# Kernel optimization log

Hardware: AMD Instinct MI355X
Metric: run time of the kernel (lower is better)

## Reference

```python
import jax, jax.numpy as jnp
import numpy as np

B, T, C, H = 2, 2048, 2048, 16
HD = C // H  # head dim = 128
ROPE_BASE = 10000.0


def apply_rope(x):
    # x: [B, T, H, HD]; interleaved-pair rotation as in torchtune RoPE
    t = x.shape[1]
    half = x.shape[-1] // 2
    theta = 1.0 / (ROPE_BASE ** (jnp.arange(0, HD, 2, dtype=jnp.float32) / HD))  # [HD/2]
    ang = jnp.arange(t, dtype=jnp.float32)[:, None] * theta[None, :]  # [T, HD/2]
    cos = jnp.cos(ang)[None, :, None, :]  # [1, T, 1, HD/2]
    sin = jnp.sin(ang)[None, :, None, :]
    xs = x.reshape(*x.shape[:-1], half, 2)  # [B,T,H,HD/2,2]
    x0, x1 = xs[..., 0], xs[..., 1]
    out = jnp.stack([x0 * cos - x1 * sin, x1 * cos + x0 * sin], axis=-1)
    return out.reshape(x.shape)


def setup_inputs() -> dict:
    key = jax.random.key(0)
    k1, k2, k3 = jax.random.split(key, 3)
    x = jax.random.normal(k1, (B, T, C), dtype=jnp.float32)
    attn_mask = jnp.tril(jnp.ones((T, T), dtype=bool))[None, None]  # causal [1,1,T,T]
    W_attn = jax.random.normal(k2, (3 * C, C), dtype=jnp.float32) * (C ** -0.5)
    W_proj = jax.random.normal(k3, (C, C), dtype=jnp.float32) * (C ** -0.5)
    return {"x": x, "attn_mask": attn_mask, "W_attn": W_attn, "W_proj": W_proj}


def reference(x, attn_mask, W_attn, W_proj):
    b, t, c = x.shape
    qkv = x @ W_attn.T  # [B,T,3C]
    q, k, v = jnp.split(qkv, 3, axis=-1)
    q = apply_rope(q.reshape(b, t, H, HD)).transpose(0, 2, 1, 3)  # [B,H,T,HD]
    k = apply_rope(k.reshape(b, t, H, HD)).transpose(0, 2, 1, 3)
    v = v.reshape(b, t, H, HD).transpose(0, 2, 1, 3)
    scale = 1.0 / jnp.sqrt(jnp.float32(HD))
    scores = jnp.einsum("bhqd,bhkd->bhqk", q, k) * scale
    scores = jnp.where(attn_mask, scores, jnp.finfo(scores.dtype).min)
    probs = jax.nn.softmax(scores, axis=-1)
    y = jnp.einsum("bhqk,bhkd->bhqd", probs, v)  # [B,H,T,HD]
    y = y.transpose(0, 2, 1, 3).reshape(b, t, c)
    return y @ W_proj.T
```

## Files before the change

kernel.cpp:

```cpp
#include <hip/hip_runtime.h>
#include <hip/hip_bf16.h>
#include <math.h>

typedef unsigned short u16;
typedef unsigned int   u32;
typedef __attribute__((ext_vector_type(8)))  short bf16x8;
typedef __attribute__((ext_vector_type(4)))  float f32x4;
typedef __attribute__((ext_vector_type(16))) float f32x16;

#define B_  2
#define T_  2048
#define C_  2048
#define H_  16
#define HD_ 128
#define M_  4096
#define N3C 6144

__device__ __forceinline__ float bf2f_lo(u32 u) { return __uint_as_float(u << 16); }
__device__ __forceinline__ float bf2f_hi(u32 u) { return __uint_as_float(u & 0xffff0000u); }

__device__ __forceinline__ u16 f2bf(float f) {
    u32 u = __float_as_uint(f);
    return (u16)((u + 0x7fffu + ((u >> 16) & 1u)) >> 16);
}
__device__ __forceinline__ u32 pack2(float a, float b) {
    return (u32)f2bf(a) | ((u32)f2bf(b) << 16);
}
__device__ __forceinline__ void store1(float* p, float v) { *p = v; }
__device__ __forceinline__ void store1(__hip_bfloat16* p, float v) { *(u16*)p = f2bf(v); }

__device__ __forceinline__ void gload16(const void* g, void* l) {
    __builtin_amdgcn_global_load_lds((__attribute__((address_space(1))) void*)g,
                                     (__attribute__((address_space(3))) void*)l, 16, 0, 0);
}

__global__ __launch_bounds__(256) void cvt_bf16(const float* __restrict__ in,
                                                u16* __restrict__ out, int n8) {
    const int i = blockIdx.x * 256 + threadIdx.x;
    if (i < n8) {
        const float4 a = ((const float4*)in)[2 * i];
        const float4 b = ((const float4*)in)[2 * i + 1];
        ((uint4*)out)[i] = make_uint4(pack2(a.x, a.y), pack2(a.z, a.w),
                                      pack2(b.x, b.y), pack2(b.z, b.w));
    }
}

template <typename TO>
__global__ __launch_bounds__(256) void gemm_lds(const __hip_bfloat16* __restrict__ A,
                                                const __hip_bfloat16* __restrict__ W,
                                                TO* __restrict__ Cout,
                                                int N, int K, int gx) {
    __shared__ u16 As[128 * 32];
    __shared__ u16 Bs[128 * 32];
    const int nwg = gridDim.x * gridDim.y;
    const int id  = blockIdx.y * gx + blockIdx.x;
    const int swz = (id & 7) * (nwg >> 3) + (id >> 3);
    const int bm  = (swz / gx) * 128;
    const int bn  = (swz % gx) * 128;

    const int tid  = threadIdx.x;
    const int w    = tid >> 6;
    const int lane = tid & 63;
    const int g    = lane >> 4;
    const int c    = lane & 15;
    const int wr   = (w >> 1) * 64;
    const int wc   = (w & 1) * 64;

    const int srow = lane >> 2;
    const int scol = (lane & 3) * 8;
    const __hip_bfloat16* ga0 = A + (size_t)(bm + w * 32 + srow) * K + scol;
    const __hip_bfloat16* ga1 = ga0 + (size_t)16 * K;
    const __hip_bfloat16* gb0 = W + (size_t)(bn + w * 32 + srow) * K + scol;
    const __hip_bfloat16* gb1 = gb0 + (size_t)16 * K;
    u16* la0 = &As[(w * 32) * 32];
    u16* la1 = &As[(w * 32 + 16) * 32];
    u16* lb0 = &Bs[(w * 32) * 32];
    u16* lb1 = &Bs[(w * 32 + 16) * 32];

    f32x4 acc[4][4];
#pragma unroll
    for (int mi = 0; mi < 4; ++mi)
#pragma unroll
        for (int ni = 0; ni < 4; ++ni)
            acc[mi][ni] = (f32x4){0.f, 0.f, 0.f, 0.f};

    for (int k0 = 0; k0 < K; k0 += 32) {
        __syncthreads();
        gload16(ga0 + k0, la0);
        gload16(ga1 + k0, la1);
        gload16(gb0 + k0, lb0);
        gload16(gb1 + k0, lb1);
        __syncthreads();

        bf16x8 af[4], bfr[4];
#pragma unroll
        for (int mi = 0; mi < 4; ++mi)
            af[mi] = *(const bf16x8*)&As[(wr + mi * 16 + c) * 32 + g * 8];
#pragma unroll
        for (int ni = 0; ni < 4; ++ni)
            bfr[ni] = *(const bf16x8*)&Bs[(wc + ni * 16 + c) * 32 + g * 8];
#pragma unroll
        for (int mi = 0; mi < 4; ++mi)
#pragma unroll
            for (int ni = 0; ni < 4; ++ni)
                acc[mi][ni] = __builtin_amdgcn_mfma_f32_16x16x32_bf16(
                    af[mi], bfr[ni], acc[mi][ni], 0, 0, 0);
    }

#pragma unroll
    for (int mi = 0; mi < 4; ++mi)
#pragma unroll
        for (int ni = 0; ni < 4; ++ni)
#pragma unroll
            for (int i = 0; i < 4; ++i) {
                const int row = bm + wr + mi * 16 + 4 * g + i;
                const int col = bn + wc + ni * 16 + c;
                store1(Cout + (size_t)row * N + col, acc[mi][ni][i]);
            }
}

__device__ __forceinline__ void stage_tile(u16* dst, const float* src, int ldk, int tid) {
    const int r0  = tid >> 3;
    const int off = (tid & 7) * 4;
#pragma unroll
    for (int it = 0; it < 4; ++it) {
        const int row = r0 + it * 32;
        const float4 v = *(const float4*)(src + (size_t)row * ldk + off);
        *(uint2*)&dst[row * 40 + off] = make_uint2(pack2(v.x, v.y), pack2(v.z, v.w));
    }
}
__device__ __forceinline__ void stage_tile(u16* dst, const __hip_bfloat16* src, int ldk, int tid) {
    const int r0  = tid >> 2;
    const int off = (tid & 3) * 8;
#pragma unroll
    for (int it = 0; it < 2; ++it) {
        const int row = r0 + it * 64;
        *(uint4*)&dst[row * 40 + off] = *(const uint4*)(src + (size_t)row * ldk + off);
    }
}

template <typename TA, typename TW, typename TO>
__global__ __launch_bounds__(256) void gemm_mfma(const TA* __restrict__ A,
                                                 const TW* __restrict__ W,
                                                 TO* __restrict__ Cout,
                                                 int N, int K, int gx) {
    __shared__ u16 As[128 * 40];
    __shared__ u16 Bs[128 * 40];
    const int nwg = gridDim.x * gridDim.y;
    const int id  = blockIdx.y * gx + blockIdx.x;
    const int swz = (id & 7) * (nwg >> 3) + (id >> 3);
    const int bm  = (swz / gx) * 128;
    const int bn  = (swz % gx) * 128;

    const int tid  = threadIdx.x;
    const int w    = tid >> 6;
    const int lane = tid & 63;
    const int g    = lane >> 4;
    const int c    = lane & 15;
    const int wr   = (w >> 1) * 64;
    const int wc   = (w & 1) * 64;

    f32x4 acc[4][4];
#pragma unroll
    for (int mi = 0; mi < 4; ++mi)
#pragma unroll
        for (int ni = 0; ni < 4; ++ni)
            acc[mi][ni] = (f32x4){0.f, 0.f, 0.f, 0.f};

    const TA* Ab = A + (size_t)bm * K;
    const TW* Wb = W + (size_t)bn * K;

    for (int k0 = 0; k0 < K; k0 += 32) {
        __syncthreads();
        stage_tile(As, Ab + k0, K, tid);
        stage_tile(Bs, Wb + k0, K, tid);
        __syncthreads();

        bf16x8 af[4], bfr[4];
#pragma unroll
        for (int mi = 0; mi < 4; ++mi)
            af[mi] = *(const bf16x8*)&As[(wr + mi * 16 + c) * 40 + g * 8];
#pragma unroll
        for (int ni = 0; ni < 4; ++ni)
            bfr[ni] = *(const bf16x8*)&Bs[(wc + ni * 16 + c) * 40 + g * 8];
#pragma unroll
        for (int mi = 0; mi < 4; ++mi)
#pragma unroll
            for (int ni = 0; ni < 4; ++ni)
                acc[mi][ni] = __builtin_amdgcn_mfma_f32_16x16x32_bf16(
                    af[mi], bfr[ni], acc[mi][ni], 0, 0, 0);
    }

#pragma unroll
    for (int mi = 0; mi < 4; ++mi)
#pragma unroll
        for (int ni = 0; ni < 4; ++ni)
#pragma unroll
            for (int i = 0; i < 4; ++i) {
                const int row = bm + wr + mi * 16 + 4 * g + i;
                const int col = bn + wc + ni * 16 + c;
                store1(Cout + (size_t)row * N + col, acc[mi][ni][i]);
            }
}

__global__ __launch_bounds__(256) void rope_kernel(__hip_bfloat16* __restrict__ qkv) {
    const int id  = blockIdx.x * 256 + threadIdx.x;
    const int i   = id & 63;
    const int h   = (id >> 6) & (H_ - 1);
    const int qk  = (id >> 10) & 1;
    const int row = id >> 11;
    const int t   = row & (T_ - 1);
    const size_t base = (size_t)row * N3C + (size_t)qk * C_ + h * HD_ + 2 * i;
    u32* p = (u32*)((u16*)qkv + base);
    const u32 v = *p;
    const float x0 = bf2f_lo(v), x1 = bf2f_hi(v);
    const float l2th = 0.20762050593046f;
    const float theta = exp2f(-(float)i * l2th);
    const float ang = (float)t * theta;
    float s, cc;
    sincosf(ang, &s, &cc);
    *p = pack2(x0 * cc - x1 * s, x1 * cc + x0 * s);
}

__device__ __forceinline__ int PI_(int s) {
    return (s & 51) | ((s & 4) << 1) | ((s & 8) >> 1);
}

__global__ __launch_bounds__(256, 2) void attn_mfma2(const __hip_bfloat16* __restrict__ qkv,
                                                     __hip_bfloat16* __restrict__ y) {
    __shared__ u16 Ks[64 * 136];
    __shared__ u16 Vt[128 * 72];
    __shared__ float Red[128];

    const int tid  = threadIdx.x;
    const int w    = tid >> 6;
    const int lane = tid & 63;
    const int c31  = lane & 31;
    const int hi   = lane >> 5;
    const int bid  = blockIdx.x;
    const int bh   = bid & 31;
    const int qb   = 15 - (bid >> 5);
    const int b    = bh >> 4, h = bh & 15;
    const int q0   = qb * 128;

    const size_t base = (size_t)b * T_ * N3C + (size_t)h * HD_;
    const __hip_bfloat16* Qp = qkv + base;
    const __hip_bfloat16* Kp = qkv + base + C_;
    const __hip_bfloat16* Vp = qkv + base + 2 * C_;

    bf16x8 qf[8];
    {
        const size_t qoff = (size_t)(q0 + w * 32 + c31) * N3C + hi * 8;
#pragma unroll
        for (int kc = 0; kc < 8; ++kc)
            qf[kc] = *(const bf16x8*)(Qp + qoff + kc * 16);
    }

    f32x16 o[4];
#pragma unroll
    for (int db = 0; db < 4; ++db)
#pragma unroll
        for (int r = 0; r < 16; ++r) o[db][r] = 0.f;

    float m_ = -1e30f, l_ = 0.f;
    const int   myq   = q0 + w * 32 + c31;
    const float SCALE = 0.08838834764831845f;

    const int s_   = tid >> 2;
    const int dsub = tid & 3;
    const int vcol = PI_(s_) ^ (dsub << 4);

    const int nkt = 2 * qb + 2;
    for (int kt = 0; kt < nkt; ++kt) {
        const int k0 = kt * 64;
        __syncthreads();
#pragma unroll
        for (int it = 0; it < 4; ++it) {
            const int col = dsub * 32 + it * 8;
            const size_t goff = (size_t)(k0 + s_) * N3C + col;
            *(uint4*)&Ks[s_ * 136 + col] = *(const uint4*)(Kp + goff);
            const uint4 vv = *(const uint4*)(Vp + goff);
            const u32 vw[4] = {vv.x, vv.y, vv.z, vv.w};
#pragma unroll
            for (int j = 0; j < 8; ++j)
                Vt[(col + j) * 72 + vcol] = (u16)(vw[j >> 1] >> ((j & 1) * 16));
        }
        __syncthreads();

        f32x16 sA, sB;
#pragma unroll
        for (int r = 0; r < 16; ++r) { sA[r] = 0.f; sB[r] = 0.f; }
#pragma unroll
        for (int kc = 0; kc < 8; ++kc) {
            const bf16x8 ka = *(const bf16x8*)&Ks[c31 * 136 + kc * 16 + hi * 8];
            sA = __builtin_amdgcn_mfma_f32_32x32x16_bf16(ka, qf[kc], sA, 0, 0, 0);
            const bf16x8 kb_ = *(const bf16x8*)&Ks[(32 + c31) * 136 + kc * 16 + hi * 8];
            sB = __builtin_amdgcn_mfma_f32_32x32x16_bf16(kb_, qf[kc], sB, 0, 0, 0);
        }

        float pmax = -1e30f;
#pragma unroll
        for (int r = 0; r < 16; ++r) {
            const int cr = (r & 3) + 8 * (r >> 2) + 4 * hi;
            sA[r] = (k0 + cr      <= myq) ? sA[r] * SCALE : -1e30f;
            sB[r] = (k0 + 32 + cr <= myq) ? sB[r] * SCALE : -1e30f;
            pmax = fmaxf(pmax, fmaxf(sA[r], sB[r]));
        }
        pmax = fmaxf(pmax, __shfl_xor(pmax, 32));

        if (__any(pmax > m_ + 8.f)) {
            const float mn   = fmaxf(m_, pmax);
            const float corr = __expf(m_ - mn);
            Red[w * 32 + c31] = corr;
            float cf[16];
#pragma unroll
            for (int r = 0; r < 16; ++r)
                cf[r] = Red[w * 32 + ((r & 3) + 8 * (r >> 2) + 4 * hi)];
#pragma unroll
            for (int db = 0; db < 4; ++db)
#pragma unroll
                for (int r = 0; r < 16; ++r) o[db][r] *= cf[r];
            l_ *= corr;
            m_ = mn;
        }

        float psum = 0.f;
#pragma unroll
        for (int r = 0; r < 16; ++r) {
            sA[r] = __expf(sA[r] - m_); psum += sA[r];
            sB[r] = __expf(sB[r] - m_); psum += sB[r];
        }
        psum += __shfl_xor(psum, 32);
        l_ += psum;

#pragma unroll
        for (int kb2 = 0; kb2 < 2; ++kb2) {
#pragma unroll
            for (int c2 = 0; c2 < 2; ++c2) {
                union { u32 u[4]; bf16x8 v; } pk;
#pragma unroll
                for (int q2 = 0; q2 < 4; ++q2) {
                    const int r = 8 * c2 + 2 * q2;
                    const float e0 = kb2 ? sB[r]     : sA[r];
                    const float e1 = kb2 ? sB[r + 1] : sA[r + 1];
                    pk.u[q2] = pack2(e0, e1);
                }
#pragma unroll
                for (int db = 0; db < 4; ++db) {
                    const int colb = (kb2 * 32 + c2 * 16 + hi * 8) ^ (db << 4);
                    const bf16x8 vb = *(const bf16x8*)&Vt[(db * 32 + c31) * 72 + colb];
                    o[db] = __builtin_amdgcn_mfma_f32_32x32x16_bf16(pk.v, vb, o[db], 0, 0, 0);
                }
            }
        }
    }

    Red[w * 32 + c31] = l_;
    float lv[16];
#pragma unroll
    for (int r = 0; r < 16; ++r)
        lv[r] = 1.f / Red[w * 32 + ((r & 3) + 8 * (r >> 2) + 4 * hi)];
#pragma unroll
    for (int db = 0; db < 4; ++db)
#pragma unroll
        for (int r = 0; r < 16; ++r) {
            const int q = q0 + w * 32 + (r & 3) + 8 * (r >> 2) + 4 * hi;
            store1(y + (size_t)(b * T_ + q) * C_ + h * HD_ + db * 32 + c31,
                   o[db][r] * lv[r]);
        }
}

extern "C" void kernel_launch(void* const* d_in, const int* in_sizes, int n_in,
                              void* d_out, int out_size, void* d_ws, size_t ws_size,
                              hipStream_t stream) {
    const float* x  = (const float*)d_in[0];
    const float* Wa = (const float*)d_in[2];
    const float* Wp = (const float*)d_in[3];
    float* out = (float*)d_out;

    u16* ws = (u16*)d_ws;
    __hip_bfloat16* qkv = (__hip_bfloat16*)ws;
    __hip_bfloat16* y   = (__hip_bfloat16*)(ws + (size_t)M_ * N3C);

    const size_t NEED = ((size_t)M_ * N3C + (size_t)M_ * C_ +
                         (size_t)M_ * C_ +
                         (size_t)N3C * C_ + (size_t)C_ * C_) * 2;

    if (ws_size >= NEED) {
        u16* xb  = ws + (size_t)M_ * N3C + (size_t)M_ * C_;
        u16* Wab = xb + (size_t)M_ * C_;
        u16* Wpb = Wab + (size_t)N3C * C_;

        cvt_bf16<<<(M_ * C_ / 8 + 255) / 256, 256, 0, stream>>>(x, xb, M_ * C_ / 8);
        cvt_bf16<<<(N3C * C_ / 8 + 255) / 256, 256, 0, stream>>>(Wa, Wab, N3C * C_ / 8);
        cvt_bf16<<<(C_ * C_ / 8 + 255) / 256, 256, 0, stream>>>(Wp, Wpb, C_ * C_ / 8);

        gemm_lds<__hip_bfloat16>
            <<<dim3(N3C / 128, M_ / 128), 256, 0, stream>>>(
                (const __hip_bfloat16*)xb, (const __hip_bfloat16*)Wab, qkv, N3C, C_, N3C / 128);
        rope_kernel<<<(M_ * C_) / 256, 256, 0, stream>>>(qkv);
        attn_mfma2<<<512, 256, 0, stream>>>(qkv, y);
        gemm_lds<float>
            <<<dim3(C_ / 128, M_ / 128), 256, 0, stream>>>(
                y, (const __hip_bfloat16*)Wpb, out, C_, C_, C_ / 128);
    } else {
        gemm_mfma<float, float, __hip_bfloat16>
            <<<dim3(N3C / 128, M_ / 128), 256, 0, stream>>>(x, Wa, qkv, N3C, C_, N3C / 128);
        rope_kernel<<<(M_ * C_) / 256, 256, 0, stream>>>(qkv);
        attn_mfma2<<<512, 256, 0, stream>>>(qkv, y);
        gemm_mfma<__hip_bfloat16, float, float>
            <<<dim3(C_ / 128, M_ / 128), 256, 0, stream>>>(y, Wp, out, C_, C_, C_ / 128);
    }
}
```

Before: 323.0 us.

## Triple-buffer GEMM LDS loads and register-prefetch K/V tiles in attention

The GEMM becomes a three-stage LDS pipeline using async global_load_lds. Loads run two tiles ahead, synchronised by explicit vmcnt waits and a single barrier per iteration, so global latency overlaps the MFMA work. The attention kernel prefetches the next K/V tile into registers while the current tile is consumed, and raises wave priority around the MFMA blocks. The cost is more LDS (three buffers) and more registers, which may lower occupancy, and correctness now depends on the hand-placed waitcnt values matching the number of outstanding loads.

```diff
diff --git a/kernel.cpp b/kernel.cpp
--- a/kernel.cpp
+++ b/kernel.cpp
@@ -46,12 +46,12 @@
 }
 
 template <typename TO>
-__global__ __launch_bounds__(256) void gemm_lds(const __hip_bfloat16* __restrict__ A,
-                                                const __hip_bfloat16* __restrict__ W,
-                                                TO* __restrict__ Cout,
-                                                int N, int K, int gx) {
-    __shared__ u16 As[128 * 32];
-    __shared__ u16 Bs[128 * 32];
+__global__ __launch_bounds__(256, 3) void gemm_pipe(const __hip_bfloat16* __restrict__ A,
+                                                    const __hip_bfloat16* __restrict__ W,
+                                                    TO* __restrict__ Cout,
+                                                    int N, int K, int gx) {
+    __shared__ u16 As[3][128 * 32];
+    __shared__ u16 Bs[3][128 * 32];
     const int nwg = gridDim.x * gridDim.y;
     const int id  = blockIdx.y * gx + blockIdx.x;
     const int swz = (id & 7) * (nwg >> 3) + (id >> 3);
@@ -72,10 +72,13 @@
     const __hip_bfloat16* ga1 = ga0 + (size_t)16 * K;
     const __hip_bfloat16* gb0 = W + (size_t)(bn + w * 32 + srow) * K + scol;
     const __hip_bfloat16* gb1 = gb0 + (size_t)16 * K;
-    u16* la0 = &As[(w * 32) * 32];
-    u16* la1 = &As[(w * 32 + 16) * 32];
-    u16* lb0 = &Bs[(w * 32) * 32];
-    u16* lb1 = &Bs[(w * 32 + 16) * 32];
+
+#define STAGE_(bi, kk) do {                                   \
+        gload16(ga0 + (kk), &As[bi][w * 1024]);               \
+        gload16(ga1 + (kk), &As[bi][w * 1024 + 512]);         \
+        gload16(gb0 + (kk), &Bs[bi][w * 1024]);               \
+        gload16(gb1 + (kk), &Bs[bi][w * 1024 + 512]);         \
+    } while (0)
 
     f32x4 acc[4][4];
 #pragma unroll
@@ -84,28 +87,43 @@
         for (int ni = 0; ni < 4; ++ni)
             acc[mi][ni] = (f32x4){0.f, 0.f, 0.f, 0.f};
 
-    for (int k0 = 0; k0 < K; k0 += 32) {
-        __syncthreads();
-        gload16(ga0 + k0, la0);
-        gload16(ga1 + k0, la1);
-        gload16(gb0 + k0, lb0);
-        gload16(gb1 + k0, lb1);
-        __syncthreads();
+    const int NT = K / 32;
+    STAGE_(0, 0);
+    STAGE_(1, 32);
+
+    int cur = 0;
+    for (int t = 0; t < NT; ++t) {
+        if (t + 1 < NT) { asm volatile("s_waitcnt vmcnt(4)" ::: "memory"); }
+        else            { asm volatile("s_waitcnt vmcnt(0)" ::: "memory"); }
+        __builtin_amdgcn_sched_barrier(0);
+        __builtin_amdgcn_s_barrier();
+        __builtin_amdgcn_sched_barrier(0);
+
+        if (t + 2 < NT) {
+            const int nb = (cur + 2 >= 3) ? cur - 1 : cur + 2;
+            STAGE_(nb, (t + 2) * 32);
+        }
 
         bf16x8 af[4], bfr[4];
 #pragma unroll
         for (int mi = 0; mi < 4; ++mi)
-            af[mi] = *(const bf16x8*)&As[(wr + mi * 16 + c) * 32 + g * 8];
-#pragma unroll
-        for (int ni = 0; ni < 4; ++ni)
-            bfr[ni] = *(const bf16x8*)&Bs[(wc + ni * 16 + c) * 32 + g * 8];
+            af[mi] = *(const bf16x8*)&As[cur][(wr + mi * 16 + c) * 32 + g * 8];
+#pragma unroll
+        for (int ni = 0; ni < 4; ++ni)
+            bfr[ni] = *(const bf16x8*)&Bs[cur][(wc + ni * 16 + c) * 32 + g * 8];
+
+        __builtin_amdgcn_s_setprio(1);
 #pragma unroll
         for (int mi = 0; mi < 4; ++mi)
 #pragma unroll
             for (int ni = 0; ni < 4; ++ni)
                 acc[mi][ni] = __builtin_amdgcn_mfma_f32_16x16x32_bf16(
                     af[mi], bfr[ni], acc[mi][ni], 0, 0, 0);
-    }
+        __builtin_amdgcn_s_setprio(0);
+
+        cur = (cur + 1 == 3) ? 0 : cur + 1;
+    }
+#undef STAGE_
 
 #pragma unroll
     for (int mi = 0; mi < 4; ++mi)
@@ -270,26 +288,43 @@
     const int dsub = tid & 3;
     const int vcol = PI_(s_) ^ (dsub << 4);
 
+    uint4 kreg[4], vreg[4];
+#pragma unroll
+    for (int it = 0; it < 4; ++it) {
+        const int col = dsub * 32 + it * 8;
+        const size_t goff = (size_t)s_ * N3C + col;
+        kreg[it] = *(const uint4*)(Kp + goff);
+        vreg[it] = *(const uint4*)(Vp + goff);
+    }
+
     const int nkt = 2 * qb + 2;
     for (int kt = 0; kt < nkt; ++kt) {
-        const int k0 = kt * 64;
         __syncthreads();
 #pragma unroll
         for (int it = 0; it < 4; ++it) {
             const int col = dsub * 32 + it * 8;
-            const size_t goff = (size_t)(k0 + s_) * N3C + col;
-            *(uint4*)&Ks[s_ * 136 + col] = *(const uint4*)(Kp + goff);
-            const uint4 vv = *(const uint4*)(Vp + goff);
-            const u32 vw[4] = {vv.x, vv.y, vv.z, vv.w};
+            *(uint4*)&Ks[s_ * 136 + col] = kreg[it];
+            const u32 vw[4] = {vreg[it].x, vreg[it].y, vreg[it].z, vreg[it].w};
 #pragma unroll
             for (int j = 0; j < 8; ++j)
                 Vt[(col + j) * 72 + vcol] = (u16)(vw[j >> 1] >> ((j & 1) * 16));
         }
+        if (kt + 1 < nkt) {
+#pragma unroll
+            for (int it = 0; it < 4; ++it) {
+                const int col = dsub * 32 + it * 8;
+                const size_t goff = (size_t)((kt + 1) * 64 + s_) * N3C + col;
+                kreg[it] = *(const uint4*)(Kp + goff);
+                vreg[it] = *(const uint4*)(Vp + goff);
+            }
+        }
         __syncthreads();
 
+        const int k0 = kt * 64;
         f32x16 sA, sB;
 #pragma unroll
         for (int r = 0; r < 16; ++r) { sA[r] = 0.f; sB[r] = 0.f; }
+        __builtin_amdgcn_s_setprio(1);
 #pragma unroll
         for (int kc = 0; kc < 8; ++kc) {
             const bf16x8 ka = *(const bf16x8*)&Ks[c31 * 136 + kc * 16 + hi * 8];
@@ -297,6 +332,7 @@
             const bf16x8 kb_ = *(const bf16x8*)&Ks[(32 + c31) * 136 + kc * 16 + hi * 8];
             sB = __builtin_amdgcn_mfma_f32_32x32x16_bf16(kb_, qf[kc], sB, 0, 0, 0);
         }
+        __builtin_amdgcn_s_setprio(0);
 
         float pmax = -1e30f;
 #pragma unroll
@@ -333,6 +369,7 @@
         psum += __shfl_xor(psum, 32);
         l_ += psum;
 
+        __builtin_amdgcn_s_setprio(1);
 #pragma unroll
         for (int kb2 = 0; kb2 < 2; ++kb2) {
 #pragma unroll
@@ -353,6 +390,7 @@
                 }
             }
         }
+        __builtin_amdgcn_s_setprio(0);
     }
 
     Red[w * 32 + c31] = l_;
@@ -395,12 +433,12 @@
         cvt_bf16<<<(N3C * C_ / 8 + 255) / 256, 256, 0, stream>>>(Wa, Wab, N3C * C_ / 8);
         cvt_bf16<<<(C_ * C_ / 8 + 255) / 256, 256, 0, stream>>>(Wp, Wpb, C_ * C_ / 8);
 
-        gemm_lds<__hip_bfloat16>
+        gemm_pipe<__hip_bfloat16>
             <<<dim3(N3C / 128, M_ / 128), 256, 0, stream>>>(
                 (const __hip_bfloat16*)xb, (const __hip_bfloat16*)Wab, qkv, N3C, C_, N3C / 128);
         rope_kernel<<<(M_ * C_) / 256, 256, 0, stream>>>(qkv);
         attn_mfma2<<<512, 256, 0, stream>>>(qkv, y);
-        gemm_lds<float>
+        gemm_pipe<float>
             <<<dim3(C_ / 128, M_ / 128), 256, 0, stream>>>(
                 y, (const __hip_bfloat16*)Wpb, out, C_, C_, C_ / 128);
     } else {
```

New measurement: 307.3 us. 4.9% less time.
